# Performance work log

Hardware: AMD Instinct MI355X
Metric: run time of the kernel (lower is better)

The kernel has to match this reference:

```python
import math
import jax, jax.numpy as jnp
import numpy as np

D = 1024      # d_model
H = 16        # n_heads
HD = 64       # head_dim
DKV = D // 2  # 512
KVHD = DKV // H  # 32
HID = D // 8  # 128 (tau/delta hidden)
B, L, F = 2, 2048, 32


def setup_inputs() -> dict:
    key = jax.random.key(0)
    ks = jax.random.split(key, 16)
    s = 0.02
    return {
        "h": jax.random.normal(ks[0], (B, L, D), jnp.float32),
        "pre_norm_mu": jax.random.normal(ks[1], (B, L, F), jnp.float32),
        "pre_norm_sigma": jax.random.uniform(ks[2], (B, L, F), jnp.float32),
        "Wq": jax.random.normal(ks[3], (D, D), jnp.float32) * s,
        "Wk": jax.random.normal(ks[4], (D, DKV), jnp.float32) * s,
        "Wv": jax.random.normal(ks[5], (D, DKV), jnp.float32) * s,
        "Wo": jax.random.normal(ks[6], (DKV, D), jnp.float32) * s,
        "bo": jnp.zeros((D,), jnp.float32),
        "tau_w1": jax.random.normal(ks[7], (D + 1, HID), jnp.float32) * s,
        "tau_b1": jnp.zeros((HID,), jnp.float32),
        "tau_w2": jax.random.normal(ks[8], (HID, 1), jnp.float32) * s,
        "tau_b2": jnp.zeros((1,), jnp.float32),
        "del_w1": jax.random.normal(ks[9], (D + 1, HID), jnp.float32) * s,
        "del_b1": jnp.zeros((HID,), jnp.float32),
        "del_w2": jax.random.normal(ks[10], (HID, DKV), jnp.float32) * s,
        "del_b2": jnp.zeros((DKV,), jnp.float32),
    }


def _mlp(x, w1, b1, w2, b2):
    # Linear -> exact GELU -> Linear (matches torch nn.GELU default)
    return jax.nn.gelu(x @ w1 + b1, approximate=False) @ w2 + b2


def reference(h, pre_norm_mu, pre_norm_sigma, Wq, Wk, Wv, Wo, bo,
              tau_w1, tau_b1, tau_w2, tau_b2, del_w1, del_b1, del_w2, del_b2):
    b, l, _ = h.shape
    sigma_mean = jnp.clip(pre_norm_sigma.mean(axis=-1, keepdims=True), 1e-6, None)  # (B,L,1)
    mu_mean = pre_norm_mu.mean(axis=-1, keepdims=True)                               # (B,L,1)

    tau = jnp.exp(jnp.clip(_mlp(jnp.concatenate([sigma_mean, h], -1),
                                tau_w1, tau_b1, tau_w2, tau_b2), -3.0, 3.0))  # (B,L,1)
    delta = jnp.clip(_mlp(jnp.concatenate([mu_mean, h], -1),
                          del_w1, del_b1, del_w2, del_b2), -5.0, 5.0)          # (B,L,DKV)

    Q = (h @ Wq).reshape(b, l, H, HD).transpose(0, 2, 1, 3)       # (B,H,L,HD)
    K = (h @ Wk).reshape(b, l, H, KVHD).transpose(0, 2, 1, 3)     # (B,H,L,KVHD)
    V = (h @ Wv).reshape(b, l, H, KVHD).transpose(0, 2, 1, 3)

    Qc = Q[..., :KVHD]                                            # (B,H,L,KVHD)
    logits = jnp.einsum('bhqd,bhkd->bhqk', Qc, K) / math.sqrt(KVHD)
    logits = tau[:, None] * logits                                # tau -> (B,1,L,1): per-query scale

    delta_r = delta.reshape(b, l, H, KVHD).transpose(0, 2, 1, 3)  # (B,H,L,KVHD)
    delta_last = delta_r[:, :, -1, :]                             # (B,H,KVHD)
    delta_bias = jnp.einsum('bhd,bhkd->bhk', delta_last, K)       # (B,H,L_k)
    logits = logits + delta_bias[:, :, None, :]

    logits = jnp.clip(logits, -50.0, 50.0)
    causal = jnp.triu(jnp.ones((l, l), bool), 1)
    logits = jnp.where(causal, -jnp.inf, logits)

    attn = jax.nn.softmax(logits, axis=-1)
    out = jnp.einsum('bhqk,bhkd->bhqd', attn, V)                  # (B,H,L,KVHD)
    out = out.transpose(0, 2, 1, 3).reshape(b, l, DKV)
    out = out @ Wo + bo
    return out[:, -1, :]                                          # (B,D)
```

## Files before the change

### kernel.cpp

```cpp
#include <hip/hip_runtime.h>
#include <hip/hip_bf16.h>

#define Dm   1024
#define Hh   16
#define HDq  64
#define DKV  512
#define HID  128
#define Bb   2
#define Ll   2048
#define Ff   32

typedef _Float16 half8 __attribute__((ext_vector_type(8)));
typedef float f32x4 __attribute__((ext_vector_type(4)));

__device__ __forceinline__ float gelu_exact(float x) {
    return 0.5f * x * (1.0f + erff(x * 0.70710678118654752f));
}

__global__ __launch_bounds__(256) void kpart(
        const float* __restrict__ h, const float* __restrict__ Wq,
        const float* __restrict__ tw1, const float* __restrict__ dw1,
        float* __restrict__ hid_part, float* __restrict__ qc_part)
{
    const int bx = blockIdx.x, t = threadIdx.x;
    __shared__ float hl0[32], hl1[32];
    __shared__ float red0[256], red1[256];
    if (bx < 64) {
        const int which = bx >> 5, js = bx & 31;
        const float* w1 = which ? dw1 : tw1;
        if (t < 32)       hl0[t]      = h[((size_t)0 * Ll + (Ll - 1)) * Dm + js * 32 + t];
        else if (t < 64)  hl1[t - 32] = h[((size_t)1 * Ll + (Ll - 1)) * Dm + js * 32 + (t - 32)];
        __syncthreads();
        const int col = t & 127, rg = t >> 7;
        float a0 = 0.f, a1 = 0.f;
#pragma unroll
        for (int p = 0; p < 16; ++p) {
            const int row = p * 2 + rg;
            const float w = w1[(size_t)(js * 32 + row + 1) * HID + col];
            a0 += hl0[row] * w;
            a1 += hl1[row] * w;
        }
        red0[t] = a0; red1[t] = a1;
        __syncthreads();
        if (t < 128) {
            hid_part[((size_t)(0 * 2 + which) * 32 + js) * HID + t] = red0[t] + red0[t + 128];
            hid_part[((size_t)(1 * 2 + which) * 32 + js) * HID + t] = red1[t] + red1[t + 128];
        }
    } else {
        const int js = bx - 64;
        if (t < 32)       hl0[t]      = h[((size_t)0 * Ll + (Ll - 1)) * Dm + js * 32 + t];
        else if (t < 64)  hl1[t - 32] = h[((size_t)1 * Ll + (Ll - 1)) * Dm + js * 32 + (t - 32)];
        __syncthreads();
        float4 a0 = {0.f, 0.f, 0.f, 0.f}, a1 = {0.f, 0.f, 0.f, 0.f};
        const float* Wq0 = Wq + (size_t)(js * 32) * Dm + t * 4;
#pragma unroll
        for (int j = 0; j < 32; ++j) {
            float4 wq = *(const float4*)(Wq0 + (size_t)j * Dm);
            const float x0 = hl0[j], x1 = hl1[j];
            a0.x += x0 * wq.x; a0.y += x0 * wq.y; a0.z += x0 * wq.z; a0.w += x0 * wq.w;
            a1.x += x1 * wq.x; a1.y += x1 * wq.y; a1.z += x1 * wq.z; a1.w += x1 * wq.w;
        }
        const int col = t * 4;
        if ((col & 63) < 32) {
            const int c = (col >> 6) * 32 + (col & 31);
            *(float4*)(qc_part + ((size_t)0 * 32 + js) * DKV + c) = a0;
            *(float4*)(qc_part + ((size_t)1 * 32 + js) * DKV + c) = a1;
        }
    }
}

__global__ __launch_bounds__(256) void kkw2(
        const float* __restrict__ mu, const float* __restrict__ sigma,
        const float* __restrict__ tw1, const float* __restrict__ tb1,
        const float* __restrict__ tw2, const float* __restrict__ tb2,
        const float* __restrict__ dw1, const float* __restrict__ db1,
        const float* __restrict__ dw2, const float* __restrict__ db2,
        const float* __restrict__ Wk,
        const float* __restrict__ hid_part, const float* __restrict__ qc_part,
        _Float16* __restrict__ kwh16)
{
    const int jt = blockIdx.x, b = blockIdx.y;
    const int t = threadIdx.x;
    __shared__ float gh[HID];
    __shared__ float red[256];
    __shared__ float wc[DKV];
    __shared__ float kl[16][36];
    __shared__ float s_tau, s_sm, s_mm;

    if (t == 0) {
        float s = 0.f;
        for (int f = 0; f < Ff; ++f) s += sigma[((size_t)b * Ll + (Ll - 1)) * Ff + f];
        s_sm = fmaxf(s / (float)Ff, 1e-6f);
    }
    if (t == 64) {
        float s = 0.f;
        for (int f = 0; f < Ff; ++f) s += mu[((size_t)b * Ll + (Ll - 1)) * Ff + f];
        s_mm = s / (float)Ff;
    }
    __syncthreads();

    if (t < 128) {
        float a = tb1[t] + s_sm * tw1[t];
#pragma unroll
        for (int s = 0; s < 32; ++s)
            a += hid_part[((size_t)(b * 2 + 0) * 32 + s) * HID + t];
        red[t] = gelu_exact(a) * tw2[t];
    } else {
        const int hh = t - 128;
        float a = db1[hh] + s_mm * dw1[hh];
#pragma unroll
        for (int s = 0; s < 32; ++s)
            a += hid_part[((size_t)(b * 2 + 1) * 32 + s) * HID + hh];
        gh[hh] = gelu_exact(a);
        red[t] = 0.f;
    }
    __syncthreads();
    for (int s = 128; s > 0; s >>= 1) {
        if (t < s) red[t] += red[t + s];
        __syncthreads();
    }
    if (t == 0) {
        float s = red[0] + tb2[0];
        s_tau = expf(fminf(fmaxf(s, -3.f), 3.f));
    }
    __syncthreads();

    const int c0 = t, c1 = t + 256;
    float d0 = db2[c0], d1 = db2[c1];
#pragma unroll 16
    for (int i = 0; i < HID; ++i) {
        const float x = gh[i];
        d0 += x * dw2[(size_t)i * DKV + c0];
        d1 += x * dw2[(size_t)i * DKV + c1];
    }
    d0 = fminf(fmaxf(d0, -5.f), 5.f);
    d1 = fminf(fmaxf(d1, -5.f), 5.f);
    float q0 = 0.f, q1 = 0.f;
#pragma unroll
    for (int s = 0; s < 32; ++s) {
        const float* qp = qc_part + ((size_t)b * 32 + s) * DKV;
        q0 += qp[c0];
        q1 += qp[c1];
    }
    const float inv_sqrt = 0.17677669529663687f;
    wc[c0] = s_tau * q0 * inv_sqrt + d0;
    wc[c1] = s_tau * q1 * inv_sqrt + d1;
    __syncthreads();

    const float w0 = wc[t * 2], w1v = wc[t * 2 + 1];
    const int hd = t >> 4;
#pragma unroll 4
    for (int jj = 0; jj < 32; ++jj) {
        const int j = jt * 32 + jj;
        float2 kv = *(const float2*)(Wk + (size_t)j * DKV + t * 2);
        float p = kv.x * w0 + kv.y * w1v;
        p += __shfl_xor(p, 1); p += __shfl_xor(p, 2);
        p += __shfl_xor(p, 4); p += __shfl_xor(p, 8);
        if ((t & 15) == 0) kl[hd][jj] = p;
    }
    __syncthreads();
    if (t < 64) {
        const int head = t & 15, jl = (t >> 4) * 8;
        half8 v;
#pragma unroll
        for (int e = 0; e < 8; ++e) v[e] = (_Float16)kl[head][jl + e];
        *(half8*)(kwh16 + ((size_t)(b * 32 + jt)) * 512 + t * 8) = v;
    }
}

__global__ __launch_bounds__(256) void kmid(
        const float* __restrict__ h, const _Float16* __restrict__ kwh16,
        float* __restrict__ den_part, float* __restrict__ hbar_part)
{
    __shared__ __align__(16) _Float16 Kw[16384];
    __shared__ float lred[4][16][17];
    __shared__ float p_lds[16][16];
    const int rt = blockIdx.x, b = blockIdx.y;
    const int t = threadIdx.x;
    const int w = t >> 6, l = t & 63;
    const int rows0 = (b * 128 + rt) * 16;

#pragma unroll
    for (int i = 0; i < 8; ++i) {
        const int idx = i * 256 + t;
        *(half8*)(Kw + idx * 8) = *(const half8*)(kwh16 + (size_t)b * 16384 + idx * 8);
    }
    __syncthreads();

    f32x4 lacc = {};
    const float* ap = h + (size_t)(rows0 + (l & 15)) * Dm + (l >> 4) * 8;
#pragma unroll
    for (int ks = 0; ks < 8; ++ks) {
        const int kt = w * 8 + ks;
        float4 x0 = *(const float4*)(ap + kt * 32);
        float4 x1 = *(const float4*)(ap + kt * 32 + 4);
        half8 af;
        af[0] = (_Float16)x0.x; af[1] = (_Float16)x0.y; af[2] = (_Float16)x0.z; af[3] = (_Float16)x0.w;
        af[4] = (_Float16)x1.x; af[5] = (_Float16)x1.y; af[6] = (_Float16)x1.z; af[7] = (_Float16)x1.w;
        half8 kf = *(const half8*)(Kw + kt * 512 + l * 8);
        lacc = __builtin_amdgcn_mfma_f32_16x16x32_f16(af, kf, lacc, 0, 0, 0);
    }
#pragma unroll
    for (int r = 0; r < 4; ++r)
        lred[w][(l >> 4) * 4 + r][l & 15] = lacc[r];
    __syncthreads();

    {
        const int row = t >> 4, head = t & 15;
        float val = lred[0][row][head] + lred[1][row][head]
                  + lred[2][row][head] + lred[3][row][head];
        val = fminf(fmaxf(val, -50.f), 50.f);
        p_lds[row][head] = __expf(val - 50.f);
    }
    __syncthreads();

    if (t < 16) {
        float s = 0.f;
#pragma unroll
        for (int r = 0; r < 16; ++r) s += p_lds[r][t];
        den_part[((size_t)b * Hh + t) * 128 + rt] = s;
    }

    const int j0 = (t & 63) * 16;
    const int h0 = (t >> 6) * 4;
    f32x4 acc2[4][4] = {};
#pragma unroll 4
    for (int l2 = 0; l2 < 16; ++l2) {
        const float* hr = h + (size_t)(rows0 + l2) * Dm + j0;
        f32x4 hv[4];
#pragma unroll
        for (int jj = 0; jj < 4; ++jj) hv[jj] = *(const f32x4*)(hr + jj * 4);
        f32x4 pp = *(const f32x4*)(&p_lds[l2][h0]);
#pragma unroll
        for (int hh = 0; hh < 4; ++hh)
#pragma unroll
            for (int jj = 0; jj < 4; ++jj)
                acc2[jj][hh] += hv[jj] * pp[hh];
    }
#pragma unroll
    for (int hh = 0; hh < 4; ++hh) {
        float* dst = hbar_part + ((size_t)(b * 128 + rt) * Hh + h0 + hh) * Dm + j0;
#pragma unroll
        for (int jj = 0; jj < 4; ++jj)
            *(f32x4*)(dst + jj * 4) = acc2[jj][hh];
    }
}

__global__ __launch_bounds__(256) void kopre(
        const float* __restrict__ hbar_part, const float* __restrict__ Wv,
        float* __restrict__ opre_part)
{
    const int hd = blockIdx.x, b = blockIdx.y, js = blockIdx.z;
    const int t = threadIdx.x;
    __shared__ f32x4 pA[32][8];
    __shared__ float hb[128];
    __shared__ float red[256];

    const int slot = t >> 3, rs = t & 7;
    f32x4 a = {};
#pragma unroll
    for (int i = 0; i < 16; ++i) {
        const int rt = rs + i * 8;
        a += *(const f32x4*)(hbar_part + ((size_t)(b * 128 + rt) * Hh + hd) * Dm + js * 128 + slot * 4);
    }
    pA[slot][rs] = a;
    __syncthreads();
    if (t < 32) {
        f32x4 s = {};
#pragma unroll
        for (int r = 0; r < 8; ++r) s += pA[t][r];
        *(f32x4*)(hb + t * 4) = s;
    }
    __syncthreads();

    const int c = t & 31, jg = t >> 5;
    float acc = 0.f;
#pragma unroll
    for (int i = 0; i < 16; ++i)
        acc += hb[jg * 16 + i] * Wv[(size_t)(js * 128 + jg * 16 + i) * DKV + hd * 32 + c];
    red[t] = acc;
    __syncthreads();
    if (t < 32) {
        float s = 0.f;
#pragma unroll
        for (int g = 0; g < 8; ++g) s += red[g * 32 + t];
        opre_part[((size_t)(b * Hh + hd) * 8 + js) * 32 + t] = s;
    }
}

__global__ __launch_bounds__(256) void kout(
        const float* __restrict__ opre_part, const float* __restrict__ den_part,
        const float* __restrict__ Wo, const float* __restrict__ bo,
        float* __restrict__ out)
{
    const int nt = blockIdx.x;
    const int t = threadIdx.x;
    __shared__ float op[2][DKV];
    __shared__ float dred[32][8];
    __shared__ float den_s[2][16];
    __shared__ float red0[256], red1[256];

    {
        const int b = t >> 7, hd = (t >> 3) & 15, rg = t & 7;
        float s = 0.f;
#pragma unroll
        for (int i = 0; i < 16; ++i)
            s += den_part[((size_t)b * Hh + hd) * 128 + rg + i * 8];
        dred[b * 16 + hd][rg] = s;
    }
    __syncthreads();
    if (t < 32) {
        float s = 0.f;
#pragma unroll
        for (int g = 0; g < 8; ++g) s += dred[t][g];
        den_s[t >> 4][t & 15] = s;
    }
    __syncthreads();
#pragma unroll
    for (int cc = 0; cc < 4; ++cc) {
        const int idx = cc * 256 + t;
        const int b = idx >> 9, c = idx & 511;
        float s = 0.f;
#pragma unroll
        for (int js = 0; js < 8; ++js)
            s += opre_part[((size_t)(b * Hh + (c >> 5)) * 8 + js) * 32 + (c & 31)];
        op[b][c] = s / den_s[b][c >> 5];
    }
    __syncthreads();

    const int nl = t & 31, cg = t >> 5;
    const int n = nt * 32 + nl;
    float a0 = 0.f, a1 = 0.f;
#pragma unroll 16
    for (int c = cg * 64; c < cg * 64 + 64; ++c) {
        const float wv = Wo[(size_t)c * Dm + n];
        a0 += op[0][c] * wv;
        a1 += op[1][c] * wv;
    }
    red0[t] = a0; red1[t] = a1;
    __syncthreads();
    if (t < 32) {
        float s0 = 0.f, s1 = 0.f;
#pragma unroll
        for (int g = 0; g < 8; ++g) { s0 += red0[g * 32 + t]; s1 += red1[g * 32 + t]; }
        const float bv = bo[nt * 32 + t];
        out[(size_t)0 * Dm + nt * 32 + t] = bv + s0;
        out[(size_t)1 * Dm + nt * 32 + t] = bv + s1;
    }
}

extern "C" void kernel_launch(void* const* d_in, const int* in_sizes, int n_in,
                              void* d_out, int out_size, void* d_ws, size_t ws_size,
                              hipStream_t stream) {
    const float* h      = (const float*)d_in[0];
    const float* mu     = (const float*)d_in[1];
    const float* sigma  = (const float*)d_in[2];
    const float* Wq     = (const float*)d_in[3];
    const float* Wk     = (const float*)d_in[4];
    const float* Wv     = (const float*)d_in[5];
    const float* Wo     = (const float*)d_in[6];
    const float* bo     = (const float*)d_in[7];
    const float* tau_w1 = (const float*)d_in[8];
    const float* tau_b1 = (const float*)d_in[9];
    const float* tau_w2 = (const float*)d_in[10];
    const float* tau_b2 = (const float*)d_in[11];
    const float* del_w1 = (const float*)d_in[12];
    const float* del_b1 = (const float*)d_in[13];
    const float* del_w2 = (const float*)d_in[14];
    const float* del_b2 = (const float*)d_in[15];
    float* out = (float*)d_out;

    _Float16* kwh16  = (_Float16*)d_ws;
    float* den_part  = (float*)(kwh16 + 32768);
    float* hid_part  = den_part + 4096;
    float* qc_part   = hid_part + 16384;
    float* opre_part = qc_part + 32768;
    float* hbar_part = opre_part + 8192;

    kpart<<<96, 256, 0, stream>>>(h, Wq, tau_w1, del_w1, hid_part, qc_part);
    kkw2<<<dim3(32, Bb), 256, 0, stream>>>(mu, sigma, tau_w1, tau_b1, tau_w2, tau_b2,
                                           del_w1, del_b1, del_w2, del_b2, Wk,
                                           hid_part, qc_part, kwh16);
    kmid<<<dim3(128, Bb), 256, 0, stream>>>(h, kwh16, den_part, hbar_part);
    kopre<<<dim3(16, Bb, 8), 256, 0, stream>>>(hbar_part, Wv, opre_part);
    kout<<<32, 256, 0, stream>>>(opre_part, den_part, Wo, bo, out);
}
```

Measured before the change: 56.13 us.

## Double row tile in kmid, split columns across blocks, widen kout grid

```diff
diff --git a/kernel.cpp b/kernel.cpp
--- a/kernel.cpp
+++ b/kernel.cpp
@@ -173,12 +173,13 @@
         float* __restrict__ den_part, float* __restrict__ hbar_part)
 {
     __shared__ __align__(16) _Float16 Kw[16384];
-    __shared__ float lred[4][16][17];
-    __shared__ float p_lds[16][16];
-    const int rt = blockIdx.x, b = blockIdx.y;
+    __shared__ float lred[4][32][17];
+    __shared__ float p_lds[32][16];
+    const int bx = blockIdx.x, b = blockIdx.y;
+    const int rt = bx >> 1, jh = bx & 1;
     const int t = threadIdx.x;
     const int w = t >> 6, l = t & 63;
-    const int rows0 = (b * 128 + rt) * 16;
+    const int rows0 = (b * 64 + rt) * 32;
 
 #pragma unroll
     for (int i = 0; i < 8; ++i) {
@@ -187,26 +188,33 @@
     }
     __syncthreads();
 
-    f32x4 lacc = {};
+    f32x4 lacc[2] = {};
     const float* ap = h + (size_t)(rows0 + (l & 15)) * Dm + (l >> 4) * 8;
 #pragma unroll
-    for (int ks = 0; ks < 8; ++ks) {
-        const int kt = w * 8 + ks;
-        float4 x0 = *(const float4*)(ap + kt * 32);
-        float4 x1 = *(const float4*)(ap + kt * 32 + 4);
-        half8 af;
-        af[0] = (_Float16)x0.x; af[1] = (_Float16)x0.y; af[2] = (_Float16)x0.z; af[3] = (_Float16)x0.w;
-        af[4] = (_Float16)x1.x; af[5] = (_Float16)x1.y; af[6] = (_Float16)x1.z; af[7] = (_Float16)x1.w;
-        half8 kf = *(const half8*)(Kw + kt * 512 + l * 8);
-        lacc = __builtin_amdgcn_mfma_f32_16x16x32_f16(af, kf, lacc, 0, 0, 0);
-    }
-#pragma unroll
-    for (int r = 0; r < 4; ++r)
-        lred[w][(l >> 4) * 4 + r][l & 15] = lacc[r];
-    __syncthreads();
-
-    {
-        const int row = t >> 4, head = t & 15;
+    for (int mt = 0; mt < 2; ++mt) {
+        const float* apm = ap + (size_t)mt * 16 * Dm;
+#pragma unroll
+        for (int ks = 0; ks < 8; ++ks) {
+            const int kt = w * 8 + ks;
+            float4 x0 = *(const float4*)(apm + kt * 32);
+            float4 x1 = *(const float4*)(apm + kt * 32 + 4);
+            half8 af;
+            af[0] = (_Float16)x0.x; af[1] = (_Float16)x0.y; af[2] = (_Float16)x0.z; af[3] = (_Float16)x0.w;
+            af[4] = (_Float16)x1.x; af[5] = (_Float16)x1.y; af[6] = (_Float16)x1.z; af[7] = (_Float16)x1.w;
+            half8 kf = *(const half8*)(Kw + kt * 512 + l * 8);
+            lacc[mt] = __builtin_amdgcn_mfma_f32_16x16x32_f16(af, kf, lacc[mt], 0, 0, 0);
+        }
+    }
+#pragma unroll
+    for (int mt = 0; mt < 2; ++mt)
+#pragma unroll
+        for (int r = 0; r < 4; ++r)
+            lred[w][mt * 16 + (l >> 4) * 4 + r][l & 15] = lacc[mt][r];
+    __syncthreads();
+
+#pragma unroll
+    for (int i = 0; i < 2; ++i) {
+        const int row = i * 16 + (t >> 4), head = t & 15;
         float val = lred[0][row][head] + lred[1][row][head]
                   + lred[2][row][head] + lred[3][row][head];
         val = fminf(fmaxf(val, -50.f), 50.f);
@@ -214,35 +222,33 @@
     }
     __syncthreads();
 
-    if (t < 16) {
-        float s = 0.f;
-#pragma unroll
-        for (int r = 0; r < 16; ++r) s += p_lds[r][t];
-        den_part[((size_t)b * Hh + t) * 128 + rt] = s;
-    }
-
-    const int j0 = (t & 63) * 16;
+    if (jh == 0 && t < 16) {
+        float s = 0.f;
+#pragma unroll
+        for (int r = 0; r < 32; ++r) s += p_lds[r][t];
+        den_part[((size_t)b * Hh + t) * 64 + rt] = s;
+    }
+
+    const int j0 = jh * 512 + (t & 63) * 8;
     const int h0 = (t >> 6) * 4;
-    f32x4 acc2[4][4] = {};
+    f32x4 acc2[2][4] = {};
 #pragma unroll 4
-    for (int l2 = 0; l2 < 16; ++l2) {
+    for (int l2 = 0; l2 < 32; ++l2) {
         const float* hr = h + (size_t)(rows0 + l2) * Dm + j0;
-        f32x4 hv[4];
-#pragma unroll
-        for (int jj = 0; jj < 4; ++jj) hv[jj] = *(const f32x4*)(hr + jj * 4);
+        f32x4 hv0 = *(const f32x4*)hr;
+        f32x4 hv1 = *(const f32x4*)(hr + 4);
         f32x4 pp = *(const f32x4*)(&p_lds[l2][h0]);
 #pragma unroll
-        for (int hh = 0; hh < 4; ++hh)
-#pragma unroll
-            for (int jj = 0; jj < 4; ++jj)
-                acc2[jj][hh] += hv[jj] * pp[hh];
+        for (int hh = 0; hh < 4; ++hh) {
+            acc2[0][hh] += hv0 * pp[hh];
+            acc2[1][hh] += hv1 * pp[hh];
+        }
     }
 #pragma unroll
     for (int hh = 0; hh < 4; ++hh) {
-        float* dst = hbar_part + ((size_t)(b * 128 + rt) * Hh + h0 + hh) * Dm + j0;
-#pragma unroll
-        for (int jj = 0; jj < 4; ++jj)
-            *(f32x4*)(dst + jj * 4) = acc2[jj][hh];
+        float* dst = hbar_part + ((size_t)(b * 64 + rt) * Hh + h0 + hh) * Dm + j0;
+        *(f32x4*)dst = acc2[0][hh];
+        *(f32x4*)(dst + 4) = acc2[1][hh];
     }
 }
 
@@ -259,9 +265,9 @@
     const int slot = t >> 3, rs = t & 7;
     f32x4 a = {};
 #pragma unroll
-    for (int i = 0; i < 16; ++i) {
+    for (int i = 0; i < 8; ++i) {
         const int rt = rs + i * 8;
-        a += *(const f32x4*)(hbar_part + ((size_t)(b * 128 + rt) * Hh + hd) * Dm + js * 128 + slot * 4);
+        a += *(const f32x4*)(hbar_part + ((size_t)(b * 64 + rt) * Hh + hd) * Dm + js * 128 + slot * 4);
     }
     pA[slot][rs] = a;
     __syncthreads();
@@ -304,8 +310,8 @@
         const int b = t >> 7, hd = (t >> 3) & 15, rg = t & 7;
         float s = 0.f;
 #pragma unroll
-        for (int i = 0; i < 16; ++i)
-            s += den_part[((size_t)b * Hh + hd) * 128 + rg + i * 8];
+        for (int i = 0; i < 8; ++i)
+            s += den_part[((size_t)b * Hh + hd) * 64 + rg + i * 8];
         dred[b * 16 + hd][rg] = s;
     }
     __syncthreads();
@@ -328,24 +334,24 @@
     }
     __syncthreads();
 
-    const int nl = t & 31, cg = t >> 5;
-    const int n = nt * 32 + nl;
+    const int nl = t & 15, cg = t >> 4;
+    const int n = nt * 16 + nl;
     float a0 = 0.f, a1 = 0.f;
-#pragma unroll 16
-    for (int c = cg * 64; c < cg * 64 + 64; ++c) {
+#pragma unroll 8
+    for (int c = cg * 32; c < cg * 32 + 32; ++c) {
         const float wv = Wo[(size_t)c * Dm + n];
         a0 += op[0][c] * wv;
         a1 += op[1][c] * wv;
     }
     red0[t] = a0; red1[t] = a1;
     __syncthreads();
-    if (t < 32) {
+    if (t < 16) {
         float s0 = 0.f, s1 = 0.f;
 #pragma unroll
-        for (int g = 0; g < 8; ++g) { s0 += red0[g * 32 + t]; s1 += red1[g * 32 + t]; }
-        const float bv = bo[nt * 32 + t];
-        out[(size_t)0 * Dm + nt * 32 + t] = bv + s0;
-        out[(size_t)1 * Dm + nt * 32 + t] = bv + s1;
+        for (int g = 0; g < 16; ++g) { s0 += red0[g * 16 + t]; s1 += red1[g * 16 + t]; }
+        const float bv = bo[nt * 16 + t];
+        out[(size_t)0 * Dm + nt * 16 + t] = bv + s0;
+        out[(size_t)1 * Dm + nt * 16 + t] = bv + s1;
     }
 }
 
@@ -372,7 +378,7 @@
 
     _Float16* kwh16  = (_Float16*)d_ws;
     float* den_part  = (float*)(kwh16 + 32768);
-    float* hid_part  = den_part + 4096;
+    float* hid_part  = den_part + 2048;
     float* qc_part   = hid_part + 16384;
     float* opre_part = qc_part + 32768;
     float* hbar_part = opre_part + 8192;
@@ -383,5 +389,5 @@
                                            hid_part, qc_part, kwh16);
     kmid<<<dim3(128, Bb), 256, 0, stream>>>(h, kwh16, den_part, hbar_part);
     kopre<<<dim3(16, Bb, 8), 256, 0, stream>>>(hbar_part, Wv, opre_part);
-    kout<<<32, 256, 0, stream>>>(opre_part, den_part, Wo, bo, out);
-}
+    kout<<<64, 256, 0, stream>>>(opre_part, den_part, Wo, bo, out);
+}
```

Result: faster. 52.24 us (-6.9%).

## Fuse prep kernels, use per-tile max softmax, store hbar partials in fp16

Applied to the files above, without the earlier changes.

```diff
diff --git a/kernel.cpp b/kernel.cpp
--- a/kernel.cpp
+++ b/kernel.cpp
@@ -11,82 +11,39 @@
 #define Ff   32
 
 typedef _Float16 half8 __attribute__((ext_vector_type(8)));
+typedef _Float16 half4v __attribute__((ext_vector_type(4)));
 typedef float f32x4 __attribute__((ext_vector_type(4)));
 
 __device__ __forceinline__ float gelu_exact(float x) {
     return 0.5f * x * (1.0f + erff(x * 0.70710678118654752f));
 }
 
-__global__ __launch_bounds__(256) void kpart(
-        const float* __restrict__ h, const float* __restrict__ Wq,
-        const float* __restrict__ tw1, const float* __restrict__ dw1,
-        float* __restrict__ hid_part, float* __restrict__ qc_part)
-{
-    const int bx = blockIdx.x, t = threadIdx.x;
-    __shared__ float hl0[32], hl1[32];
-    __shared__ float red0[256], red1[256];
-    if (bx < 64) {
-        const int which = bx >> 5, js = bx & 31;
-        const float* w1 = which ? dw1 : tw1;
-        if (t < 32)       hl0[t]      = h[((size_t)0 * Ll + (Ll - 1)) * Dm + js * 32 + t];
-        else if (t < 64)  hl1[t - 32] = h[((size_t)1 * Ll + (Ll - 1)) * Dm + js * 32 + (t - 32)];
-        __syncthreads();
-        const int col = t & 127, rg = t >> 7;
-        float a0 = 0.f, a1 = 0.f;
-#pragma unroll
-        for (int p = 0; p < 16; ++p) {
-            const int row = p * 2 + rg;
-            const float w = w1[(size_t)(js * 32 + row + 1) * HID + col];
-            a0 += hl0[row] * w;
-            a1 += hl1[row] * w;
-        }
-        red0[t] = a0; red1[t] = a1;
-        __syncthreads();
-        if (t < 128) {
-            hid_part[((size_t)(0 * 2 + which) * 32 + js) * HID + t] = red0[t] + red0[t + 128];
-            hid_part[((size_t)(1 * 2 + which) * 32 + js) * HID + t] = red1[t] + red1[t + 128];
-        }
-    } else {
-        const int js = bx - 64;
-        if (t < 32)       hl0[t]      = h[((size_t)0 * Ll + (Ll - 1)) * Dm + js * 32 + t];
-        else if (t < 64)  hl1[t - 32] = h[((size_t)1 * Ll + (Ll - 1)) * Dm + js * 32 + (t - 32)];
-        __syncthreads();
-        float4 a0 = {0.f, 0.f, 0.f, 0.f}, a1 = {0.f, 0.f, 0.f, 0.f};
-        const float* Wq0 = Wq + (size_t)(js * 32) * Dm + t * 4;
-#pragma unroll
-        for (int j = 0; j < 32; ++j) {
-            float4 wq = *(const float4*)(Wq0 + (size_t)j * Dm);
-            const float x0 = hl0[j], x1 = hl1[j];
-            a0.x += x0 * wq.x; a0.y += x0 * wq.y; a0.z += x0 * wq.z; a0.w += x0 * wq.w;
-            a1.x += x1 * wq.x; a1.y += x1 * wq.y; a1.z += x1 * wq.z; a1.w += x1 * wq.w;
-        }
-        const int col = t * 4;
-        if ((col & 63) < 32) {
-            const int c = (col >> 6) * 32 + (col & 31);
-            *(float4*)(qc_part + ((size_t)0 * 32 + js) * DKV + c) = a0;
-            *(float4*)(qc_part + ((size_t)1 * 32 + js) * DKV + c) = a1;
-        }
-    }
-}
-
-__global__ __launch_bounds__(256) void kkw2(
+__global__ __launch_bounds__(256) void kprep2(
+        const float* __restrict__ h,
         const float* __restrict__ mu, const float* __restrict__ sigma,
+        const float* __restrict__ Wq, const float* __restrict__ Wk,
         const float* __restrict__ tw1, const float* __restrict__ tb1,
         const float* __restrict__ tw2, const float* __restrict__ tb2,
         const float* __restrict__ dw1, const float* __restrict__ db1,
         const float* __restrict__ dw2, const float* __restrict__ db2,
-        const float* __restrict__ Wk,
-        const float* __restrict__ hid_part, const float* __restrict__ qc_part,
         _Float16* __restrict__ kwh16)
 {
     const int jt = blockIdx.x, b = blockIdx.y;
     const int t = threadIdx.x;
+    __shared__ float hl[Dm];
+    __shared__ float red[256];
+    __shared__ float redB[256];
+    __shared__ f32x4 qpart[128];
     __shared__ float gh[HID];
-    __shared__ float red[256];
+    __shared__ float qc[DKV];
     __shared__ float wc[DKV];
     __shared__ float kl[16][36];
     __shared__ float s_tau, s_sm, s_mm;
 
+    {
+        float4 v = *(const float4*)(h + ((size_t)b * Ll + (Ll - 1)) * Dm + t * 4);
+        *(float4*)(hl + t * 4) = v;
+    }
     if (t == 0) {
         float s = 0.f;
         for (int f = 0; f < Ff; ++f) s += sigma[((size_t)b * Ll + (Ll - 1)) * Ff + f];
@@ -99,21 +56,28 @@
     }
     __syncthreads();
 
+    const int col = t & 127, rg = t >> 7;
+    {
+        float at = 0.f, ad = 0.f;
+        const int j0 = rg * 512;
+#pragma unroll 8
+        for (int i = 0; i < 512; ++i) {
+            const float x = hl[j0 + i];
+            at += x * tw1[(size_t)(j0 + i + 1) * HID + col];
+            ad += x * dw1[(size_t)(j0 + i + 1) * HID + col];
+        }
+        red[t] = at; redB[t] = ad;
+    }
+    __syncthreads();
+    float tauterm = 0.f;
     if (t < 128) {
-        float a = tb1[t] + s_sm * tw1[t];
-#pragma unroll
-        for (int s = 0; s < 32; ++s)
-            a += hid_part[((size_t)(b * 2 + 0) * 32 + s) * HID + t];
-        red[t] = gelu_exact(a) * tw2[t];
-    } else {
-        const int hh = t - 128;
-        float a = db1[hh] + s_mm * dw1[hh];
-#pragma unroll
-        for (int s = 0; s < 32; ++s)
-            a += hid_part[((size_t)(b * 2 + 1) * 32 + s) * HID + hh];
-        gh[hh] = gelu_exact(a);
-        red[t] = 0.f;
-    }
+        float a  = red[t] + red[t + 128] + tb1[t] + s_sm * tw1[t];
+        float ad = redB[t] + redB[t + 128] + db1[t] + s_mm * dw1[t];
+        gh[t] = gelu_exact(ad);
+        tauterm = gelu_exact(a) * tw2[t];
+    }
+    __syncthreads();
+    red[t] = (t < 128) ? tauterm : 0.f;
     __syncthreads();
     for (int s = 128; s > 0; s >>= 1) {
         if (t < s) red[t] += red[t + s];
@@ -123,28 +87,42 @@
         float s = red[0] + tb2[0];
         s_tau = expf(fminf(fmaxf(s, -3.f), 3.f));
     }
-    __syncthreads();
-
-    const int c0 = t, c1 = t + 256;
-    float d0 = db2[c0], d1 = db2[c1];
+
+    {
+        const int q = t & 127, rh = t >> 7;
+        const int colq = (q >> 3) * HDq + (q & 7) * 4;
+        f32x4 aq = {};
+        const int j0 = rh * 512;
+#pragma unroll 8
+        for (int i = 0; i < 512; ++i) {
+            const float x = hl[j0 + i];
+            f32x4 wq = *(const f32x4*)(Wq + (size_t)(j0 + i) * Dm + colq);
+            aq += x * wq;
+        }
+        if (rh == 1) qpart[q] = aq;
+        __syncthreads();
+        if (rh == 0) {
+            f32x4 s = aq + qpart[q];
+            *(f32x4*)(qc + q * 4) = s;
+        }
+    }
+    __syncthreads();
+
+    {
+        const int c0 = t, c1 = t + 256;
+        float d0 = db2[c0], d1 = db2[c1];
 #pragma unroll 16
-    for (int i = 0; i < HID; ++i) {
-        const float x = gh[i];
-        d0 += x * dw2[(size_t)i * DKV + c0];
-        d1 += x * dw2[(size_t)i * DKV + c1];
-    }
-    d0 = fminf(fmaxf(d0, -5.f), 5.f);
-    d1 = fminf(fmaxf(d1, -5.f), 5.f);
-    float q0 = 0.f, q1 = 0.f;
-#pragma unroll
-    for (int s = 0; s < 32; ++s) {
-        const float* qp = qc_part + ((size_t)b * 32 + s) * DKV;
-        q0 += qp[c0];
-        q1 += qp[c1];
-    }
-    const float inv_sqrt = 0.17677669529663687f;
-    wc[c0] = s_tau * q0 * inv_sqrt + d0;
-    wc[c1] = s_tau * q1 * inv_sqrt + d1;
+        for (int i = 0; i < HID; ++i) {
+            const float x = gh[i];
+            d0 += x * dw2[(size_t)i * DKV + c0];
+            d1 += x * dw2[(size_t)i * DKV + c1];
+        }
+        d0 = fminf(fmaxf(d0, -5.f), 5.f);
+        d1 = fminf(fmaxf(d1, -5.f), 5.f);
+        const float inv_sqrt = 0.17677669529663687f;
+        wc[c0] = s_tau * qc[c0] * inv_sqrt + d0;
+        wc[c1] = s_tau * qc[c1] * inv_sqrt + d1;
+    }
     __syncthreads();
 
     const float w0 = wc[t * 2], w1v = wc[t * 2 + 1];
@@ -170,11 +148,13 @@
 
 __global__ __launch_bounds__(256) void kmid(
         const float* __restrict__ h, const _Float16* __restrict__ kwh16,
-        float* __restrict__ den_part, float* __restrict__ hbar_part)
+        float* __restrict__ m_part, float* __restrict__ den_part,
+        _Float16* __restrict__ hbar16)
 {
     __shared__ __align__(16) _Float16 Kw[16384];
     __shared__ float lred[4][16][17];
     __shared__ float p_lds[16][16];
+    __shared__ float m_s[16];
     const int rt = blockIdx.x, b = blockIdx.y;
     const int t = threadIdx.x;
     const int w = t >> 6, l = t & 63;
@@ -210,10 +190,22 @@
         float val = lred[0][row][head] + lred[1][row][head]
                   + lred[2][row][head] + lred[3][row][head];
         val = fminf(fmaxf(val, -50.f), 50.f);
-        p_lds[row][head] = __expf(val - 50.f);
-    }
-    __syncthreads();
-
+        p_lds[row][head] = val;
+    }
+    __syncthreads();
+    if (t < 16) {
+        float m = -1e30f;
+#pragma unroll
+        for (int r = 0; r < 16; ++r) m = fmaxf(m, p_lds[r][t]);
+        m_s[t] = m;
+        m_part[((size_t)b * Hh + t) * 128 + rt] = m;
+    }
+    __syncthreads();
+    {
+        const int row = t >> 4, head = t & 15;
+        p_lds[row][head] = __expf(p_lds[row][head] - m_s[head]);
+    }
+    __syncthreads();
     if (t < 16) {
         float s = 0.f;
 #pragma unroll
@@ -239,29 +231,54 @@
     }
 #pragma unroll
     for (int hh = 0; hh < 4; ++hh) {
-        float* dst = hbar_part + ((size_t)(b * 128 + rt) * Hh + h0 + hh) * Dm + j0;
-#pragma unroll
-        for (int jj = 0; jj < 4; ++jj)
-            *(f32x4*)(dst + jj * 4) = acc2[jj][hh];
+        _Float16* dst = hbar16 + ((size_t)(b * 128 + rt) * Hh + h0 + hh) * Dm + j0;
+        half8 v0, v1;
+#pragma unroll
+        for (int e = 0; e < 4; ++e) {
+            v0[e]     = (_Float16)acc2[0][hh][e];
+            v0[e + 4] = (_Float16)acc2[1][hh][e];
+            v1[e]     = (_Float16)acc2[2][hh][e];
+            v1[e + 4] = (_Float16)acc2[3][hh][e];
+        }
+        *(half8*)dst = v0;
+        *(half8*)(dst + 8) = v1;
     }
 }
 
 __global__ __launch_bounds__(256) void kopre(
-        const float* __restrict__ hbar_part, const float* __restrict__ Wv,
-        float* __restrict__ opre_part)
+        const _Float16* __restrict__ hbar16, const float* __restrict__ m_part,
+        const float* __restrict__ Wv, float* __restrict__ opre_part)
 {
     const int hd = blockIdx.x, b = blockIdx.y, js = blockIdx.z;
     const int t = threadIdx.x;
     __shared__ f32x4 pA[32][8];
     __shared__ float hb[128];
     __shared__ float red[256];
+    __shared__ float w_s[128];
+    __shared__ float Msh;
+
+    float mt = -1e30f;
+    if (t < 128) mt = m_part[((size_t)b * Hh + hd) * 128 + t];
+    red[t] = mt;
+    __syncthreads();
+    for (int s = 128; s > 0; s >>= 1) {
+        if (t < s) red[t] = fmaxf(red[t], red[t + s]);
+        __syncthreads();
+    }
+    if (t == 0) Msh = red[0];
+    __syncthreads();
+    if (t < 128) w_s[t] = __expf(mt - Msh);
+    __syncthreads();
 
     const int slot = t >> 3, rs = t & 7;
     f32x4 a = {};
 #pragma unroll
     for (int i = 0; i < 16; ++i) {
         const int rt = rs + i * 8;
-        a += *(const f32x4*)(hbar_part + ((size_t)(b * 128 + rt) * Hh + hd) * Dm + js * 128 + slot * 4);
+        half4v v = *(const half4v*)(hbar16 + ((size_t)(b * 128 + rt) * Hh + hd) * Dm + js * 128 + slot * 4);
+        const float wt = w_s[rt];
+        a[0] += wt * (float)v[0]; a[1] += wt * (float)v[1];
+        a[2] += wt * (float)v[2]; a[3] += wt * (float)v[3];
     }
     pA[slot][rs] = a;
     __syncthreads();
@@ -289,7 +306,8 @@
 }
 
 __global__ __launch_bounds__(256) void kout(
-        const float* __restrict__ opre_part, const float* __restrict__ den_part,
+        const float* __restrict__ opre_part, const float* __restrict__ m_part,
+        const float* __restrict__ den_part,
         const float* __restrict__ Wo, const float* __restrict__ bo,
         float* __restrict__ out)
 {
@@ -297,16 +315,37 @@
     const int t = threadIdx.x;
     __shared__ float op[2][DKV];
     __shared__ float dred[32][8];
+    __shared__ float Ms[32];
     __shared__ float den_s[2][16];
     __shared__ float red0[256], red1[256];
 
-    {
-        const int b = t >> 7, hd = (t >> 3) & 15, rg = t & 7;
-        float s = 0.f;
+    const int pr = t >> 3, rg = t & 7;
+    const int pb = pr >> 4, ph = pr & 15;
+    {
+        float m = -1e30f;
 #pragma unroll
         for (int i = 0; i < 16; ++i)
-            s += den_part[((size_t)b * Hh + hd) * 128 + rg + i * 8];
-        dred[b * 16 + hd][rg] = s;
+            m = fmaxf(m, m_part[((size_t)pb * Hh + ph) * 128 + rg + i * 8]);
+        dred[pr][rg] = m;
+    }
+    __syncthreads();
+    if (t < 32) {
+        float m = -1e30f;
+#pragma unroll
+        for (int g = 0; g < 8; ++g) m = fmaxf(m, dred[t][g]);
+        Ms[t] = m;
+    }
+    __syncthreads();
+    {
+        const float M = Ms[pr];
+        float s = 0.f;
+#pragma unroll
+        for (int i = 0; i < 16; ++i) {
+            const int rt = rg + i * 8;
+            s += __expf(m_part[((size_t)pb * Hh + ph) * 128 + rt] - M)
+               * den_part[((size_t)pb * Hh + ph) * 128 + rt];
+        }
+        dred[pr][rg] = s;
     }
     __syncthreads();
     if (t < 32) {
@@ -328,24 +367,24 @@
     }
     __syncthreads();
 
-    const int nl = t & 31, cg = t >> 5;
-    const int n = nt * 32 + nl;
+    const int nl = t & 15, cg = t >> 4;
+    const int n = nt * 16 + nl;
     float a0 = 0.f, a1 = 0.f;
-#pragma unroll 16
-    for (int c = cg * 64; c < cg * 64 + 64; ++c) {
+#pragma unroll 8
+    for (int c = cg * 32; c < cg * 32 + 32; ++c) {
         const float wv = Wo[(size_t)c * Dm + n];
         a0 += op[0][c] * wv;
         a1 += op[1][c] * wv;
     }
     red0[t] = a0; red1[t] = a1;
     __syncthreads();
-    if (t < 32) {
+    if (t < 16) {
         float s0 = 0.f, s1 = 0.f;
 #pragma unroll
-        for (int g = 0; g < 8; ++g) { s0 += red0[g * 32 + t]; s1 += red1[g * 32 + t]; }
-        const float bv = bo[nt * 32 + t];
-        out[(size_t)0 * Dm + nt * 32 + t] = bv + s0;
-        out[(size_t)1 * Dm + nt * 32 + t] = bv + s1;
+        for (int g = 0; g < 16; ++g) { s0 += red0[g * 16 + t]; s1 += red1[g * 16 + t]; }
+        const float bv = bo[nt * 16 + t];
+        out[(size_t)0 * Dm + nt * 16 + t] = bv + s0;
+        out[(size_t)1 * Dm + nt * 16 + t] = bv + s1;
     }
 }
 
@@ -371,17 +410,15 @@
     float* out = (float*)d_out;
 
     _Float16* kwh16  = (_Float16*)d_ws;
-    float* den_part  = (float*)(kwh16 + 32768);
-    float* hid_part  = den_part + 4096;
-    float* qc_part   = hid_part + 16384;
-    float* opre_part = qc_part + 32768;
-    float* hbar_part = opre_part + 8192;
-
-    kpart<<<96, 256, 0, stream>>>(h, Wq, tau_w1, del_w1, hid_part, qc_part);
-    kkw2<<<dim3(32, Bb), 256, 0, stream>>>(mu, sigma, tau_w1, tau_b1, tau_w2, tau_b2,
-                                           del_w1, del_b1, del_w2, del_b2, Wk,
-                                           hid_part, qc_part, kwh16);
-    kmid<<<dim3(128, Bb), 256, 0, stream>>>(h, kwh16, den_part, hbar_part);
-    kopre<<<dim3(16, Bb, 8), 256, 0, stream>>>(hbar_part, Wv, opre_part);
-    kout<<<32, 256, 0, stream>>>(opre_part, den_part, Wo, bo, out);
-}
+    _Float16* hbar16 = kwh16 + 32768;
+    float* m_part    = (float*)(hbar16 + (size_t)2 * 128 * Hh * Dm);
+    float* den_part  = m_part + 4096;
+    float* opre_part = den_part + 4096;
+
+    kprep2<<<dim3(32, Bb), 256, 0, stream>>>(h, mu, sigma, Wq, Wk,
+                                             tau_w1, tau_b1, tau_w2, tau_b2,
+                                             del_w1, del_b1, del_w2, del_b2, kwh16);
+    kmid<<<dim3(128, Bb), 256, 0, stream>>>(h, kwh16, m_part, den_part, hbar16);
+    kopre<<<dim3(16, Bb, 8), 256, 0, stream>>>(hbar16, m_part, Wv, opre_part);
+    kout<<<64, 256, 0, stream>>>(opre_part, m_part, den_part, Wo, bo, out);
+}
```

New measurement: 94.34 us. 68.1% more time.
